# Performance work log

Hardware: AMD Instinct MI355X
Metric: run time of the kernel (lower is better)

Reference implementation:

```python
import jax, jax.numpy as jnp
import numpy as np

B, T, H, HS, E = 4096, 32, 16, 32, 512  # T == block_size == head_size (required by the module's concat-on-time quirk)


def setup_inputs() -> dict:
    key = jax.random.key(0)
    ks = jax.random.split(key, 6)
    s_e = 1.0 / np.sqrt(E).astype(np.float32)
    s_p = 1.0 / np.sqrt(H * HS).astype(np.float32)
    return {
        "x": jax.random.normal(ks[0], (B, T, E), jnp.float32),
        "Wq": jax.random.normal(ks[1], (H, HS, E), jnp.float32) * s_e,  # per-head Linear(E->HS, no bias)
        "Wk": jax.random.normal(ks[2], (H, HS, E), jnp.float32) * s_e,
        "Wv": jax.random.normal(ks[3], (H, HS, E), jnp.float32) * s_e,
        "Wp": jax.random.normal(ks[4], (E, H * HS), jnp.float32) * s_p,  # proj: Linear(H*HS -> E)
        "bp": jnp.zeros((E,), jnp.float32),
    }


def reference(x, Wq, Wk, Wv, Wp, bp):
    # Per-head projections, batched over heads (original loops in Python).
    q = jnp.einsum('bte,hde->bhtd', x, Wq)  # [B,H,T,HS]
    k = jnp.einsum('bte,hde->bhtd', x, Wk)
    v = jnp.einsum('bte,hde->bhtd', x, Wv)
    wei = jnp.einsum('bhtd,bhsd->bhts', q, k) * (HS ** -0.5)  # [B,H,T,T]
    mask = jnp.tril(jnp.ones((T, T), bool))  # causal (T == block_size)
    wei = jnp.where(mask, wei, -jnp.inf)
    wei = jax.nn.softmax(wei, axis=-1)
    # dropout is identity in eval mode
    out = jnp.einsum('bhts,bhsd->bhtd', wei, v)  # [B,H,T,HS]
    # torch.cat(..., dim=1): stack head outputs along the TIME axis -> [B, H*T, HS]
    out = out.reshape(B, H * T, HS)
    out = jnp.swapaxes(out, 1, 2)  # [B, HS, H*T]; valid only because T == HS -> last dim == H*HS == E
    return out @ Wp.T + bp  # [B, HS, E]
```

## Files before the change

kernel.cpp:

```cpp
#include <hip/hip_runtime.h>
#include <stdint.h>

typedef __attribute__((ext_vector_type(8))) short bf16x8;
typedef __attribute__((ext_vector_type(4))) float f32x4;

#define MFMA16(a, b, c) __builtin_amdgcn_mfma_f32_16x16x32_bf16((a), (b), (c), 0, 0, 0)

__device__ __forceinline__ unsigned short f2bf(float f) {
  unsigned int b = __float_as_uint(f);
  b += 0x7FFFu + ((b >> 16) & 1u);
  return (unsigned short)(b >> 16);
}
__device__ __forceinline__ bf16x8 cvt8(const float4 a, const float4 b) {
  bf16x8 r;
  r[0] = (short)f2bf(a.x); r[1] = (short)f2bf(a.y);
  r[2] = (short)f2bf(a.z); r[3] = (short)f2bf(a.w);
  r[4] = (short)f2bf(b.x); r[5] = (short)f2bf(b.y);
  r[6] = (short)f2bf(b.z); r[7] = (short)f2bf(b.w);
  return r;
}
template <bool BF16W>
__device__ __forceinline__ bf16x8 ldw(const void* p, size_t off) {
  if constexpr (BF16W) {
    return *(const bf16x8*)((const unsigned short*)p + off);
  } else {
    const float* f = (const float*)p + off;
    return cvt8(*(const float4*)f, *(const float4*)(f + 4));
  }
}
__device__ __forceinline__ int sw(int row, int chunk) {
  return row * 512 + ((chunk ^ (row & 7)) << 3);
}

__global__ void cvt_weights_k(const float* __restrict__ wq,
                              const float* __restrict__ wk,
                              const float* __restrict__ wv,
                              const float* __restrict__ wp,
                              unsigned short* __restrict__ dst) {
  const int seg = blockIdx.x >> 7;
  const int blk = blockIdx.x & 127;
  const float* src = (seg == 0) ? wq : (seg == 1) ? wk : (seg == 2) ? wv : wp;
  unsigned short* d = dst + (size_t)seg * 262144;
  const int c = blk * 256 + threadIdx.x;
  const int row = ((c >> 10) << 4) + (c & 15);
  const int col = ((c >> 6) & 15) * 32 + ((c >> 4) & 3) * 8;
  const float* s = src + row * 512 + col;
  *(bf16x8*)&d[(size_t)c * 8] = cvt8(*(const float4*)s, *(const float4*)(s + 4));
}

template <bool PACKED>
__device__ __forceinline__ size_t wbase0(int g32, int lane, int m, int quad) {
  if constexpr (PACKED) return (size_t)g32 * 512 + (size_t)lane * 8;
  else                  return (size_t)(g32 + m) * 512 + quad * 8;
}

template <bool BF16W>
__global__ __launch_bounds__(256, 3) void qkv_attn_k(
    const float* __restrict__ x,
    const void* __restrict__ wq,
    const void* __restrict__ wk,
    const void* __restrict__ wv,
    float* __restrict__ y) {
  __shared__ __align__(16) unsigned short Xs[32 * 512];
  __shared__ __align__(16) unsigned short Scr[4][2][32 * 40];
  const int tid  = threadIdx.x;
  const int lane = tid & 63;
  const int wave = tid >> 6;
  const int m    = lane & 15;
  const int quad = lane >> 4;
  const int b    = blockIdx.x;

  {
    const float* xg = x + (size_t)b * (32 * 512);
#pragma unroll
    for (int i = 0; i < 8; i++) {
      int c = tid + 256 * i;
      int row = c >> 6, ch = c & 63;
      float4 lo = *(const float4*)&xg[row * 512 + ch * 8];
      float4 hi = *(const float4*)&xg[row * 512 + ch * 8 + 4];
      *(bf16x8*)&Xs[sw(row, ch)] = cvt8(lo, hi);
    }
  }
  __syncthreads();

  unsigned short* Qs = &Scr[wave][0][0];
  unsigned short* Ks = &Scr[wave][1][0];

  for (int hg = 0; hg < 4; hg++) {
    const int h = hg * 4 + wave;
    f32x4 aq[2][2] = {}; f32x4 ak[2][2] = {}; f32x4 av[2][2] = {};
    const size_t wb = wbase0<BF16W>(h * 32, lane, m, quad);
    const int kmul = BF16W ? 512 : 32;

    bf16x8 a0A, a1A, bq0A, bq1A, bk0A, bk1A, bv0A, bv1A;
    bf16x8 a0B, a1B, bq0B, bq1B, bk0B, bk1B, bv0B, bv1B;

#define LDF(S, idx) { \
    const int kx = (idx); \
    const size_t kb = (size_t)kx * kmul; \
    a0##S  = *(const bf16x8*)&Xs[sw(m, kx * 4 + quad)]; \
    a1##S  = *(const bf16x8*)&Xs[sw(16 + m, kx * 4 + quad)]; \
    bq0##S = ldw<BF16W>(wq, wb + kb); \
    bq1##S = ldw<BF16W>(wq, wb + 8192 + kb); \
    bk0##S = ldw<BF16W>(wk, wb + kb); \
    bk1##S = ldw<BF16W>(wk, wb + 8192 + kb); \
    bv0##S = ldw<BF16W>(wv, wb + kb); \
    bv1##S = ldw<BF16W>(wv, wb + 8192 + kb); }

#define MMF(S) { \
    aq[0][0] = MFMA16(a0##S, bq0##S, aq[0][0]); \
    aq[1][0] = MFMA16(a1##S, bq0##S, aq[1][0]); \
    aq[0][1] = MFMA16(a0##S, bq1##S, aq[0][1]); \
    aq[1][1] = MFMA16(a1##S, bq1##S, aq[1][1]); \
    ak[0][0] = MFMA16(a0##S, bk0##S, ak[0][0]); \
    ak[1][0] = MFMA16(a1##S, bk0##S, ak[1][0]); \
    ak[0][1] = MFMA16(a0##S, bk1##S, ak[0][1]); \
    ak[1][1] = MFMA16(a1##S, bk1##S, ak[1][1]); \
    av[0][0] = MFMA16(a0##S, bv0##S, av[0][0]); \
    av[1][0] = MFMA16(a1##S, bv0##S, av[1][0]); \
    av[0][1] = MFMA16(a0##S, bv1##S, av[0][1]); \
    av[1][1] = MFMA16(a1##S, bv1##S, av[1][1]); }

    LDF(A, 0)
    for (int i = 0; i < 14; i += 2) {
      LDF(B, i + 1)
      MMF(A)
      LDF(A, i + 2)
      MMF(B)
    }
    LDF(B, 15)
    MMF(A)
    MMF(B)
#undef LDF
#undef MMF

#pragma unroll
    for (int mi = 0; mi < 2; mi++)
#pragma unroll
      for (int ni = 0; ni < 2; ni++)
#pragma unroll
        for (int r = 0; r < 4; r++) {
          int row = mi * 16 + quad * 4 + r;
          int col = ni * 16 + m;
          Qs[row * 40 + col] = f2bf(aq[mi][ni][r]);
          Ks[row * 40 + col] = f2bf(ak[mi][ni][r]);
        }
    f32x4 sAcc[2][2];
#pragma unroll
    for (int mi = 0; mi < 2; mi++)
#pragma unroll
      for (int ni = 0; ni < 2; ni++) {
        bf16x8 qa = *(const bf16x8*)&Qs[(mi * 16 + m) * 40 + quad * 8];
        bf16x8 kb = *(const bf16x8*)&Ks[(ni * 16 + m) * 40 + quad * 8];
        f32x4 z = {};
        sAcc[mi][ni] = MFMA16(qa, kb, z);
      }
    float invs[2][4];
#pragma unroll
    for (int mi = 0; mi < 2; mi++)
#pragma unroll
      for (int r = 0; r < 4; r++) {
        int t = mi * 16 + quad * 4 + r;
        float s0 = sAcc[mi][0][r] * 0.17677669529663687f;
        float s1 = sAcc[mi][1][r] * 0.17677669529663687f;
        s0 = (m <= t) ? s0 : -1e30f;
        s1 = (16 + m <= t) ? s1 : -1e30f;
        float mx = fmaxf(s0, s1);
#pragma unroll
        for (int off = 1; off < 16; off <<= 1) mx = fmaxf(mx, __shfl_xor(mx, off));
        float e0 = __expf(s0 - mx);
        float e1 = __expf(s1 - mx);
        float sm = e0 + e1;
#pragma unroll
        for (int off = 1; off < 16; off <<= 1) sm += __shfl_xor(sm, off);
        invs[mi][r] = 1.0f / sm;
        Qs[t * 40 + m] = f2bf(e0);
        Qs[t * 40 + 16 + m] = f2bf(e1);
      }
#pragma unroll
    for (int mi = 0; mi < 2; mi++)
#pragma unroll
      for (int ni = 0; ni < 2; ni++)
#pragma unroll
        for (int r = 0; r < 4; r++) {
          int row = mi * 16 + quad * 4 + r;
          int col = ni * 16 + m;
          Ks[col * 40 + row] = f2bf(av[mi][ni][r]);
        }
    f32x4 oAcc[2][2];
#pragma unroll
    for (int mi = 0; mi < 2; mi++)
#pragma unroll
      for (int ni = 0; ni < 2; ni++) {
        bf16x8 pa = *(const bf16x8*)&Qs[(mi * 16 + m) * 40 + quad * 8];
        bf16x8 vb = *(const bf16x8*)&Ks[(ni * 16 + m) * 40 + quad * 8];
        f32x4 z = {};
        oAcc[mi][ni] = MFMA16(pa, vb, z);
      }
#pragma unroll
    for (int mi = 0; mi < 2; mi++)
#pragma unroll
      for (int ni = 0; ni < 2; ni++) {
        float4 o;
        o.x = oAcc[mi][ni][0] * invs[mi][0];
        o.y = oAcc[mi][ni][1] * invs[mi][1];
        o.z = oAcc[mi][ni][2] * invs[mi][2];
        o.w = oAcc[mi][ni][3] * invs[mi][3];
        int d = ni * 16 + m;
        int t0 = mi * 16 + quad * 4;
        *(float4*)&y[(size_t)b * 16384 + (size_t)d * 512 + h * 32 + t0] = o;
      }
  }
}

template <bool BF16W>
__global__ __launch_bounds__(256, 2) void proj_k(
    float* __restrict__ y,
    const void* __restrict__ wp,
    const float* __restrict__ bp) {
  __shared__ __align__(16) unsigned short Ys[64 * 512];
  const int tid  = threadIdx.x;
  const int lane = tid & 63;
  const int wave = tid >> 6;
  const int m    = lane & 15;
  const int quad = lane >> 4;
  const size_t rbase = (size_t)blockIdx.x * 64;

  {
    const float* yg = y + rbase * 512;
#pragma unroll
    for (int i = 0; i < 16; i++) {
      int c = tid + 256 * i;
      int row = c >> 6, ch = c & 63;
      float4 lo = *(const float4*)&yg[row * 512 + ch * 8];
      float4 hi = *(const float4*)&yg[row * 512 + ch * 8 + 4];
      *(bf16x8*)&Ys[sw(row, ch)] = cvt8(lo, hi);
    }
  }
  __syncthreads();

  const int nb = wave * 128;
  const size_t wbp = wbase0<BF16W>(nb, lane, m, quad);
  const int kmul = BF16W ? 512 : 32;
  f32x4 acc[4][8] = {};
  bf16x8 aA[4], aB[4], wA[8], wB[8];

#define K2A(S, idx) { \
    const int kx = (idx); \
    _Pragma("unroll") \
    for (int mi = 0; mi < 4; mi++) \
      a##S[mi] = *(const bf16x8*)&Ys[sw(mi * 16 + m, kx * 4 + quad)]; }
#define K2W(S, idx) { \
    const size_t kb = (size_t)(idx) * kmul; \
    _Pragma("unroll") \
    for (int ni = 0; ni < 8; ni++) \
      w##S[ni] = ldw<BF16W>(wp, wbp + (size_t)ni * 8192 + kb); }
#define K2MM(S) { \
    _Pragma("unroll") \
    for (int ni = 0; ni < 8; ni++) \
      _Pragma("unroll") \
      for (int mi = 0; mi < 4; mi++) \
        acc[mi][ni] = MFMA16(a##S[mi], w##S[ni], acc[mi][ni]); }

  K2A(A, 0) K2W(A, 0)
  for (int i = 0; i < 14; i += 2) {
    K2A(B, i + 1) K2W(B, i + 1)
    K2MM(A)
    K2A(A, i + 2) K2W(A, i + 2)
    K2MM(B)
  }
  K2A(B, 15) K2W(B, 15)
  K2MM(A)
  K2MM(B)
#undef K2A
#undef K2W
#undef K2MM

#pragma unroll
  for (int ni = 0; ni < 8; ni++) {
    const int col = nb + ni * 16 + m;
    const float bias = bp[col];
#pragma unroll
    for (int mi = 0; mi < 4; mi++)
#pragma unroll
      for (int r = 0; r < 4; r++) {
        size_t row = rbase + mi * 16 + quad * 4 + r;
        y[row * 512 + col] = acc[mi][ni][r] + bias;
      }
  }
}

extern "C" void kernel_launch(void* const* d_in, const int* in_sizes, int n_in,
                              void* d_out, int out_size, void* d_ws, size_t ws_size,
                              hipStream_t stream) {
  (void)in_sizes; (void)n_in; (void)out_size;
  const float* x  = (const float*)d_in[0];
  const float* wq = (const float*)d_in[1];
  const float* wk = (const float*)d_in[2];
  const float* wv = (const float*)d_in[3];
  const float* wp = (const float*)d_in[4];
  const float* bp = (const float*)d_in[5];
  float* y = (float*)d_out;

  const size_t WE = 262144;
  if (ws_size >= 4 * WE * sizeof(unsigned short)) {
    unsigned short* wb = (unsigned short*)d_ws;
    cvt_weights_k<<<512, 256, 0, stream>>>(wq, wk, wv, wp, wb);
    qkv_attn_k<true><<<4096, 256, 0, stream>>>(x, wb, wb + WE, wb + 2 * WE, y);
    proj_k<true><<<2048, 256, 0, stream>>>(y, wb + 3 * WE, bp);
  } else {
    qkv_attn_k<false><<<4096, 256, 0, stream>>>(x, wq, wk, wv, y);
    proj_k<false><<<2048, 256, 0, stream>>>(y, wp, bp);
  }
}
```

Before: 1.430 ms.

## Deepen weight-load prefetch to five stages and stage V in separate LDS buffer

Replaces the two-stage double-buffered K-loop with a five-deep rotating register pipeline for the Q/K/V weight fragments, with X fragments still double-buffered from LDS. The aim is to hide global/L2 weight-load latency behind more in-flight MFMA work. V is now written transposed into its own LDS scratch buffer at the same time as Q and K, instead of reusing the K buffer after softmax. In exchange, occupancy drops from 3 to 2 blocks per SM via launch bounds, which allows more registers but gives fewer waves for latency hiding, and LDS use grows.

```diff
diff --git a/kernel.cpp b/kernel.cpp
--- a/kernel.cpp
+++ b/kernel.cpp
@@ -55,14 +55,14 @@
 }
 
 template <bool BF16W>
-__global__ __launch_bounds__(256, 3) void qkv_attn_k(
+__global__ __launch_bounds__(256, 2) void qkv_attn_k(
     const float* __restrict__ x,
     const void* __restrict__ wq,
     const void* __restrict__ wk,
     const void* __restrict__ wv,
     float* __restrict__ y) {
   __shared__ __align__(16) unsigned short Xs[32 * 512];
-  __shared__ __align__(16) unsigned short Scr[4][2][32 * 40];
+  __shared__ __align__(16) unsigned short Scr[4][3][32 * 40];
   const int tid  = threadIdx.x;
   const int lane = tid & 63;
   const int wave = tid >> 6;
@@ -85,6 +85,7 @@
 
   unsigned short* Qs = &Scr[wave][0][0];
   unsigned short* Ks = &Scr[wave][1][0];
+  unsigned short* Vt = &Scr[wave][2][0];
 
   for (int hg = 0; hg < 4; hg++) {
     const int h = hg * 4 + wave;
@@ -92,46 +93,54 @@
     const size_t wb = wbase0<BF16W>(h * 32, lane, m, quad);
     const int kmul = BF16W ? 512 : 32;
 
-    bf16x8 a0A, a1A, bq0A, bq1A, bk0A, bk1A, bv0A, bv1A;
-    bf16x8 a0B, a1B, bq0B, bq1B, bk0B, bk1B, bv0B, bv1B;
-
-#define LDF(S, idx) { \
-    const int kx = (idx); \
-    const size_t kb = (size_t)kx * kmul; \
-    a0##S  = *(const bf16x8*)&Xs[sw(m, kx * 4 + quad)]; \
-    a1##S  = *(const bf16x8*)&Xs[sw(16 + m, kx * 4 + quad)]; \
-    bq0##S = ldw<BF16W>(wq, wb + kb); \
-    bq1##S = ldw<BF16W>(wq, wb + 8192 + kb); \
-    bk0##S = ldw<BF16W>(wk, wb + kb); \
-    bk1##S = ldw<BF16W>(wk, wb + 8192 + kb); \
-    bv0##S = ldw<BF16W>(wv, wb + kb); \
-    bv1##S = ldw<BF16W>(wv, wb + 8192 + kb); }
-
-#define MMF(S) { \
-    aq[0][0] = MFMA16(a0##S, bq0##S, aq[0][0]); \
-    aq[1][0] = MFMA16(a1##S, bq0##S, aq[1][0]); \
-    aq[0][1] = MFMA16(a0##S, bq1##S, aq[0][1]); \
-    aq[1][1] = MFMA16(a1##S, bq1##S, aq[1][1]); \
-    ak[0][0] = MFMA16(a0##S, bk0##S, ak[0][0]); \
-    ak[1][0] = MFMA16(a1##S, bk0##S, ak[1][0]); \
-    ak[0][1] = MFMA16(a0##S, bk1##S, ak[0][1]); \
-    ak[1][1] = MFMA16(a1##S, bk1##S, ak[1][1]); \
-    av[0][0] = MFMA16(a0##S, bv0##S, av[0][0]); \
-    av[1][0] = MFMA16(a1##S, bv0##S, av[1][0]); \
-    av[0][1] = MFMA16(a0##S, bv1##S, av[0][1]); \
-    av[1][1] = MFMA16(a1##S, bv1##S, av[1][1]); }
-
-    LDF(A, 0)
-    for (int i = 0; i < 14; i += 2) {
-      LDF(B, i + 1)
-      MMF(A)
-      LDF(A, i + 2)
-      MMF(B)
-    }
-    LDF(B, 15)
-    MMF(A)
-    MMF(B)
-#undef LDF
+    bf16x8 q00, q10, k00, k10, v00, v10;
+    bf16x8 q01, q11, k01, k11, v01, v11;
+    bf16x8 q02, q12, k02, k12, v02, v12;
+    bf16x8 q03, q13, k03, k13, v03, v13;
+    bf16x8 q04, q14, k04, k14, v04, v14;
+    bf16x8 a0A, a1A, a0B, a1B;
+
+#define LDW(n, idx) { const size_t kb = wb + (size_t)(idx) * kmul; \
+    q0##n = ldw<BF16W>(wq, kb); q1##n = ldw<BF16W>(wq, kb + 8192); \
+    k0##n = ldw<BF16W>(wk, kb); k1##n = ldw<BF16W>(wk, kb + 8192); \
+    v0##n = ldw<BF16W>(wv, kb); v1##n = ldw<BF16W>(wv, kb + 8192); }
+#define LDA(s, idx) { \
+    a0##s = *(const bf16x8*)&Xs[sw(m, (idx) * 4 + quad)]; \
+    a1##s = *(const bf16x8*)&Xs[sw(16 + m, (idx) * 4 + quad)]; }
+#define MMF(n, s) { \
+    aq[0][0] = MFMA16(a0##s, q0##n, aq[0][0]); \
+    aq[1][0] = MFMA16(a1##s, q0##n, aq[1][0]); \
+    aq[0][1] = MFMA16(a0##s, q1##n, aq[0][1]); \
+    aq[1][1] = MFMA16(a1##s, q1##n, aq[1][1]); \
+    ak[0][0] = MFMA16(a0##s, k0##n, ak[0][0]); \
+    ak[1][0] = MFMA16(a1##s, k0##n, ak[1][0]); \
+    ak[0][1] = MFMA16(a0##s, k1##n, ak[0][1]); \
+    ak[1][1] = MFMA16(a1##s, k1##n, ak[1][1]); \
+    av[0][0] = MFMA16(a0##s, v0##n, av[0][0]); \
+    av[1][0] = MFMA16(a1##s, v0##n, av[1][0]); \
+    av[0][1] = MFMA16(a0##s, v1##n, av[0][1]); \
+    av[1][1] = MFMA16(a1##s, v1##n, av[1][1]); }
+
+    LDA(A, 0)
+    LDW(0, 0) LDW(1, 1) LDW(2, 2) LDW(3, 3) LDW(4, 4)
+    LDA(B, 1)  MMF(0, A)  LDW(0, 5)
+    LDA(A, 2)  MMF(1, B)  LDW(1, 6)
+    LDA(B, 3)  MMF(2, A)  LDW(2, 7)
+    LDA(A, 4)  MMF(3, B)  LDW(3, 8)
+    LDA(B, 5)  MMF(4, A)  LDW(4, 9)
+    LDA(A, 6)  MMF(0, B)  LDW(0, 10)
+    LDA(B, 7)  MMF(1, A)  LDW(1, 11)
+    LDA(A, 8)  MMF(2, B)  LDW(2, 12)
+    LDA(B, 9)  MMF(3, A)  LDW(3, 13)
+    LDA(A, 10) MMF(4, B)  LDW(4, 14)
+    LDA(B, 11) MMF(0, A)  LDW(0, 15)
+    LDA(A, 12) MMF(1, B)
+    LDA(B, 13) MMF(2, A)
+    LDA(A, 14) MMF(3, B)
+    LDA(B, 15) MMF(4, A)
+               MMF(0, B)
+#undef LDW
+#undef LDA
 #undef MMF
 
 #pragma unroll
@@ -144,6 +153,7 @@
           int col = ni * 16 + m;
           Qs[row * 40 + col] = f2bf(aq[mi][ni][r]);
           Ks[row * 40 + col] = f2bf(ak[mi][ni][r]);
+          Vt[col * 40 + row] = f2bf(av[mi][ni][r]);
         }
     f32x4 sAcc[2][2];
 #pragma unroll
@@ -177,23 +187,13 @@
         Qs[t * 40 + m] = f2bf(e0);
         Qs[t * 40 + 16 + m] = f2bf(e1);
       }
-#pragma unroll
-    for (int mi = 0; mi < 2; mi++)
-#pragma unroll
-      for (int ni = 0; ni < 2; ni++)
-#pragma unroll
-        for (int r = 0; r < 4; r++) {
-          int row = mi * 16 + quad * 4 + r;
-          int col = ni * 16 + m;
-          Ks[col * 40 + row] = f2bf(av[mi][ni][r]);
-        }
     f32x4 oAcc[2][2];
 #pragma unroll
     for (int mi = 0; mi < 2; mi++)
 #pragma unroll
       for (int ni = 0; ni < 2; ni++) {
         bf16x8 pa = *(const bf16x8*)&Qs[(mi * 16 + m) * 40 + quad * 8];
-        bf16x8 vb = *(const bf16x8*)&Ks[(ni * 16 + m) * 40 + quad * 8];
+        bf16x8 vb = *(const bf16x8*)&Vt[(ni * 16 + m) * 40 + quad * 8];
         f32x4 z = {};
         oAcc[mi][ni] = MFMA16(pa, vb, z);
       }
```

Measured after the change: 1.267 ms. 11.4% less time.
